# Kernel tuning notes

Measured on AMD Instinct MI355X. Metric: run time of the kernel, lower is better.

The kernel has to match this reference:

```python
import jax, jax.numpy as jnp
import numpy as np


def _count_components(img, cls):
    """Count 4-connected components of pixels equal to `cls` in a 2D int map.

    Equivalent to the numba DFS flood fill: each component is counted once.
    Implemented as min-label propagation: seed every in-class pixel with its
    linear index, iterate min over 4-neighbors (same-class only, since
    out-of-class pixels hold the sentinel BIG) until convergence; a component
    root is a pixel whose final label equals its own index.
    """
    H, W = img.shape
    BIG = H * W  # sentinel larger than any pixel index
    mask = img == cls
    idx = jnp.arange(BIG, dtype=jnp.int32).reshape(H, W)
    lab0 = jnp.where(mask, idx, BIG).astype(jnp.int32)

    def cond(state):
        return state[1]

    def body(state):
        lab, _ = state
        p = jnp.pad(lab, 1, constant_values=BIG)
        nmin = jnp.minimum(jnp.minimum(p[:-2, 1:-1], p[2:, 1:-1]),
                           jnp.minimum(p[1:-1, :-2], p[1:-1, 2:]))
        new = jnp.where(mask, jnp.minimum(lab, nmin), BIG)
        return new, jnp.any(new != lab)

    lab, _ = jax.lax.while_loop(cond, body, (lab0, jnp.array(True)))
    # roots: in-class pixels whose propagated label is their own index
    return jnp.sum(mask & (lab == idx)).astype(jnp.float32)


def _counts23(img):
    # component counts for labels 2 and 3 (the only ones the loss uses)
    return _count_components(img, 2), _count_components(img, 3)


def setup_inputs() -> dict:
    key = jax.random.key(0)
    k1, k2 = jax.random.split(key)
    pred = jax.random.normal(k1, (8, 4, 1, 768, 768), dtype=jnp.float32)
    anno = jax.random.randint(k2, (8, 1, 768, 768), 0, 4, dtype=jnp.int32)
    return {"pred": pred, "anno": anno}


def reference(pred, anno):
    # pred: [B, C, 1, H, W], anno: [B, 1, H, W]
    pred_argmax = jnp.argmax(pred, axis=1)[:, 0]  # [B, H, W] (detached semantics)
    anno_map = anno[:, 0]                          # [B, H, W]
    a2, a3 = jax.vmap(_counts23)(anno_map)
    p2, p3 = jax.vmap(_counts23)(pred_argmax)
    term2 = 1.0 - 2.0 * jnp.minimum(p2, a2) / (a2 + p2)
    term3 = 1.0 - 2.0 * jnp.minimum(p3, a3) / (a3 + p3)
    # original sums per-batch terms into connEF, then loss = connEF / 2
    return jnp.sum(term2 + term3) / 2.0
```

## Files before the change

kernel.cpp:

```cpp
#include <hip/hip_runtime.h>

#define W     768
#define PIX   (768*768)
#define NMAPS 16
#define TROWS 6
#define TPX   (TROWS*W)
#define NT    (768/TROWS)
#define NB    (NT-1)
#define NSEG  (TPX/64)
#define NIT   (NSEG/4)
#define CSLOT 16


__device__ __forceinline__ int find_root_p(volatile int* L, int x) {
    int y = L[x] >> 2;
    while (y != x) { x = y; y = L[x] >> 2; }
    return x;
}

__device__ __forceinline__ void unite_p(int* L, int a, int b, int c) {
    volatile int* Lv = L;
    while (true) {
        a = find_root_p(Lv, a);
        b = find_root_p(Lv, b);
        if (a == b) return;
        if (a > b) { int t = a; a = b; b = t; }
        int old = atomicMin(&L[b], (a << 2) | c);
        if ((old >> 2) == b) return;
        b = old >> 2;
    }
}

__device__ __forceinline__ bool unite_gp(int* L, int a, int b, int c) {
    volatile int* Lv = L;
    while (true) {
        a = find_root_p(Lv, a);
        b = find_root_p(Lv, b);
        if (a == b) return false;
        if (a > b) { int t = a; a = b; b = t; }
        int old = atomicMin(&L[b], (a << 2) | c);
        if ((old >> 2) == b) return true;
        b = old >> 2;
    }
}


__global__ __launch_bounds__(256) void fused_k(const float* __restrict__ pred,
                                               const int*   __restrict__ anno,
                                               int* __restrict__ labels,
                                               int* __restrict__ counts, int m0) {
    __shared__ int lab[TPX];
    __shared__ int s2[4], s3[4];

    int mc   = blockIdx.x / NT;
    int t    = blockIdx.x - mc * NT;
    int m    = m0 + mc;
    int tid  = threadIdx.x;
    int wid  = tid >> 6;
    int lane = tid & 63;

    unsigned long long lem = (lane == 63) ? ~0ULL : ((2ULL << lane) - 1);

    int pc[3] = {0, 0, 0};
    int pm[3] = {0, 0, 0};

    const int*   asrc = anno + (size_t)m * PIX + (size_t)t * TPX;
    const float* psrc = pred + (size_t)(m < 8 ? 0 : (m - 8)) * 4 * PIX + (size_t)t * TPX;
    bool is_anno = (m < 8);

    int   na = 0;
    float nv0 = 0.f, nv1 = 0.f, nv2 = 0.f, nv3 = 0.f;
    {
        int px = wid * 64 + lane;
        if (is_anno) {
            na = asrc[px];
        } else {
            nv0 = psrc[px];
            nv1 = psrc[(size_t)PIX + px];
            nv2 = psrc[(size_t)2 * PIX + px];
            nv3 = psrc[(size_t)3 * PIX + px];
        }
    }

    #pragma unroll
    for (int it = 0; it < NIT; ++it) {
        int seg = wid + 4 * it;
        int px  = seg * 64 + lane;
        int   ca = na;
        float v0 = nv0, v1 = nv1, v2 = nv2, v3 = nv3;
        if (it + 1 < NIT) {
            int pxn = px + 256;
            if (is_anno) {
                na = asrc[pxn];
            } else {
                nv0 = psrc[pxn];
                nv1 = psrc[(size_t)PIX + pxn];
                nv2 = psrc[(size_t)2 * PIX + pxn];
                nv3 = psrc[(size_t)3 * PIX + pxn];
            }
        }
        int c;
        if (is_anno) {
            c = ca & 3;
        } else {
            c = 0; float bv = v0;
            if (v1 > bv) { bv = v1; c = 1; }
            if (v2 > bv) { bv = v2; c = 2; }
            if (v3 > bv) { bv = v3; c = 3; }
        }
        unsigned long long blo = __ballot(c & 1);
        unsigned long long bhi = __ballot(c & 2);
        unsigned long long dif = ((blo ^ (blo << 1)) | (bhi ^ (bhi << 1))) | 1ULL;
        int ms = 63 - __clzll(dif & lem);
        lab[px] = ((seg * 64 + ms) << 2) | c;
        const int sl = it % 3;
        if (it >= 3) {
            if ((c & 2) && c == pc[sl]) {
                int mx = ms > pm[sl] ? ms : pm[sl];
                if (lane == mx) unite_p(lab, px - W, px, c);
            }
        }
        pc[sl] = c; pm[sl] = ms;
    }
    __syncthreads();

    if (tid < TROWS * 11) {
        int row = tid / 11, j = tid % 11;
        int px  = row * W + (j + 1) * 64;
        int v = lab[px], c = v & 3;
        if (c & 2) {
            int vl = lab[px - 1];
            if ((vl & 3) == c) unite_p(lab, px - 1, px, c);
        }
    }
    __syncthreads();

    int c2 = 0, c3 = 0;
    int lbase = t * TPX;
    int* gl = labels + (size_t)mc * PIX + lbase;
    #pragma unroll
    for (int it = 0; it < NIT; ++it) {
        int seg = wid + 4 * it;
        int px  = seg * 64 + lane;
        int v   = lab[px];
        int c   = v & 3;
        bool incls  = (c & 2) != 0;
        bool isroot = incls && ((v >> 2) == px);
        if (isroot) { if (c == 2) c2++; else c3++; }
        if (it < 3 || it >= NIT - 3) {
            int outv;
            if (incls) {
                int r = find_root_p(lab, px);
                outv = ((lbase + r) << 2) | c;
            } else {
                outv = ((lbase + px) << 2) | c;
            }
            gl[px] = outv;
        } else if (isroot) {
            gl[px] = ((lbase + px) << 2) | c;
        }
    }
    for (int off = 32; off; off >>= 1) {
        c2 += __shfl_down(c2, off, 64);
        c3 += __shfl_down(c3, off, 64);
    }
    if (lane == 0) { s2[wid] = c2; s3[wid] = c3; }
    __syncthreads();
    if (tid == 0) {
        int t2 = s2[0] + s2[1] + s2[2] + s2[3];
        int t3 = s3[0] + s3[1] + s3[2] + s3[3];
        if (t2) atomicAdd(&counts[(m * 2 + 0) * CSLOT], t2);
        if (t3) atomicAdd(&counts[(m * 2 + 1) * CSLOT], t3);
    }
}

__global__ __launch_bounds__(256) void boundary_k(int* __restrict__ labels,
                                                  int* __restrict__ counts, int m0) {
    __shared__ int s2[4], s3[4];
    const int HM = NB * (W / 2);
    int i    = blockIdx.x * 256 + threadIdx.x;
    int mc   = blockIdx.y;
    int m    = m0 + mc;
    int lane = threadIdx.x & 63;

    int m2 = 0, m3 = 0;
    if (i < HM) {
        int b   = i / (W / 2);
        int col = (i - b * (W / 2)) * 2;
        int* L  = labels + (size_t)mc * PIX;
        int p1  = b * TPX + (TROWS - 1) * W + col;
        int p2  = p1 + W;
        int2 va = *(const int2*)&L[p1];
        int2 vb = *(const int2*)&L[p2];
        int pay = __shfl_up(va.y, 1), pby = __shfl_up(vb.y, 1);
        int c0 = va.x & 3;
        if (c0 == (vb.x & 3) && (c0 & 2)) {
            bool red = (lane > 0) && (pay == va.x) && (pby == vb.x);
            if (!red && unite_gp(L, p1, p2, c0)) { if (c0 == 2) m2++; else m3++; }
        }
        int c1 = va.y & 3;
        if (c1 == (vb.y & 3) && (c1 & 2)) {
            bool red = (va.x == va.y) && (vb.x == vb.y);
            if (!red && unite_gp(L, p1 + 1, p2 + 1, c1)) { if (c1 == 2) m2++; else m3++; }
        }
    }
    for (int off = 32; off; off >>= 1) {
        m2 += __shfl_down(m2, off, 64);
        m3 += __shfl_down(m3, off, 64);
    }
    int wid = threadIdx.x >> 6;
    if (lane == 0) { s2[wid] = m2; s3[wid] = m3; }
    __syncthreads();
    if (threadIdx.x == 0) {
        int t2 = s2[0] + s2[1] + s2[2] + s2[3];
        int t3 = s3[0] + s3[1] + s3[2] + s3[3];
        if (t2) atomicSub(&counts[(m * 2 + 0) * CSLOT], t2);
        if (t3) atomicSub(&counts[(m * 2 + 1) * CSLOT], t3);
    }
}

__global__ void final_k(const int* __restrict__ counts, float* __restrict__ out) {
    float s = 0.0f;
    for (int b = 0; b < 8; ++b) {
        float a2 = (float)counts[(b * 2 + 0) * CSLOT];
        float a3 = (float)counts[(b * 2 + 1) * CSLOT];
        float p2 = (float)counts[((8 + b) * 2 + 0) * CSLOT];
        float p3 = (float)counts[((8 + b) * 2 + 1) * CSLOT];
        float t2 = 1.0f - 2.0f * fminf(p2, a2) / (a2 + p2);
        float t3 = 1.0f - 2.0f * fminf(p3, a3) / (a3 + p3);
        s += t2 + t3;
    }
    out[0] = 0.5f * s;
}


extern "C" void kernel_launch(void* const* d_in, const int* in_sizes, int n_in,
                              void* d_out, int out_size, void* d_ws, size_t ws_size,
                              hipStream_t stream) {
    const float* pred = (const float*)d_in[0];
    const int*   anno = (const int*)d_in[1];
    float* out = (float*)d_out;

    int* counts = (int*)d_ws;
    char* base  = (char*)d_ws + 4096;

    const size_t per_map = (size_t)PIX * 4;
    size_t avail = (ws_size > 4096) ? ws_size - 4096 : 0;
    int K = (int)(avail / per_map);
    if (K > NMAPS) K = NMAPS;
    if (K < 1)     K = 1;

    hipMemsetAsync(counts, 0, 32 * CSLOT * sizeof(int), stream);

    const int HM = NB * (W / 2);
    for (int m0 = 0; m0 < NMAPS; m0 += K) {
        int nm = NMAPS - m0; if (nm > K) nm = K;
        int* labels = (int*)base;
        fused_k   <<<dim3(nm * NT), 256, 0, stream>>>(pred, anno, labels, counts, m0);
        boundary_k<<<dim3((HM + 255) / 256, nm), 256, 0, stream>>>(labels, counts, m0);
    }
    final_k<<<1, 1, 0, stream>>>(counts, out);
}
```

Measured before the change: 57.68 us.

## Count components from run starts minus merges and write only boundary rows

Component counts are now computed during labeling: lane 0 counts the run starts of class 2 and 3 in each wavefront segment, and every successful union subtracts one. This removes the full second pass over all shared-memory pixels that looked for roots. The global label write is limited to the first and last three row-segments, plus the root entries those pixels point to. That cuts global writes, but it depends on union success being counted exactly once per merge, including under concurrent atomics.

```diff
diff --git a/kernel.cpp b/kernel.cpp
--- a/kernel.cpp
+++ b/kernel.cpp
@@ -18,20 +18,7 @@
     return x;
 }
 
-__device__ __forceinline__ void unite_p(int* L, int a, int b, int c) {
-    volatile int* Lv = L;
-    while (true) {
-        a = find_root_p(Lv, a);
-        b = find_root_p(Lv, b);
-        if (a == b) return;
-        if (a > b) { int t = a; a = b; b = t; }
-        int old = atomicMin(&L[b], (a << 2) | c);
-        if ((old >> 2) == b) return;
-        b = old >> 2;
-    }
-}
-
-__device__ __forceinline__ bool unite_gp(int* L, int a, int b, int c) {
+__device__ __forceinline__ bool unite_p(int* L, int a, int b, int c) {
     volatile int* Lv = L;
     while (true) {
         a = find_root_p(Lv, a);
@@ -63,6 +50,7 @@
 
     int pc[3] = {0, 0, 0};
     int pm[3] = {0, 0, 0};
+    int c2 = 0, c3 = 0;
 
     const int*   asrc = anno + (size_t)m * PIX + (size_t)t * TPX;
     const float* psrc = pred + (size_t)(m < 8 ? 0 : (m - 8)) * 4 * PIX + (size_t)t * TPX;
@@ -111,13 +99,19 @@
         unsigned long long blo = __ballot(c & 1);
         unsigned long long bhi = __ballot(c & 2);
         unsigned long long dif = ((blo ^ (blo << 1)) | (bhi ^ (bhi << 1))) | 1ULL;
+        if (lane == 0) {
+            c2 += (int)__popcll(dif & bhi & ~blo);
+            c3 += (int)__popcll(dif & bhi &  blo);
+        }
         int ms = 63 - __clzll(dif & lem);
         lab[px] = ((seg * 64 + ms) << 2) | c;
         const int sl = it % 3;
         if (it >= 3) {
             if ((c & 2) && c == pc[sl]) {
                 int mx = ms > pm[sl] ? ms : pm[sl];
-                if (lane == mx) unite_p(lab, px - W, px, c);
+                if (lane == mx && unite_p(lab, px - W, px, c)) {
+                    if (c == 2) c2--; else c3--;
+                }
             }
         }
         pc[sl] = c; pm[sl] = ms;
@@ -130,35 +124,28 @@
         int v = lab[px], c = v & 3;
         if (c & 2) {
             int vl = lab[px - 1];
-            if ((vl & 3) == c) unite_p(lab, px - 1, px, c);
-        }
-    }
-    __syncthreads();
-
-    int c2 = 0, c3 = 0;
+            if ((vl & 3) == c && unite_p(lab, px - 1, px, c)) {
+                if (c == 2) c2--; else c3--;
+            }
+        }
+    }
+    __syncthreads();
+
     int lbase = t * TPX;
     int* gl = labels + (size_t)mc * PIX + lbase;
     #pragma unroll
-    for (int it = 0; it < NIT; ++it) {
+    for (int q = 0; q < 6; ++q) {
+        int it  = (q < 3) ? q : (NIT - 6 + q);
         int seg = wid + 4 * it;
         int px  = seg * 64 + lane;
         int v   = lab[px];
         int c   = v & 3;
-        bool incls  = (c & 2) != 0;
-        bool isroot = incls && ((v >> 2) == px);
-        if (isroot) { if (c == 2) c2++; else c3++; }
-        if (it < 3 || it >= NIT - 3) {
-            int outv;
-            if (incls) {
-                int r = find_root_p(lab, px);
-                outv = ((lbase + r) << 2) | c;
-            } else {
-                outv = ((lbase + px) << 2) | c;
-            }
-            gl[px] = outv;
-        } else if (isroot) {
-            gl[px] = ((lbase + px) << 2) | c;
-        }
+        int r   = px;
+        if (c & 2) r = find_root_p(lab, px);
+        int rl = __shfl_up(r, 1);
+        gl[px] = ((lbase + r) << 2) | c;
+        if ((c & 2) && (lane == 0 || rl != r))
+            gl[r] = ((lbase + r) << 2) | c;
     }
     for (int off = 32; off; off >>= 1) {
         c2 += __shfl_down(c2, off, 64);
@@ -196,12 +183,12 @@
         int c0 = va.x & 3;
         if (c0 == (vb.x & 3) && (c0 & 2)) {
             bool red = (lane > 0) && (pay == va.x) && (pby == vb.x);
-            if (!red && unite_gp(L, p1, p2, c0)) { if (c0 == 2) m2++; else m3++; }
+            if (!red && unite_p(L, p1, p2, c0)) { if (c0 == 2) m2++; else m3++; }
         }
         int c1 = va.y & 3;
         if (c1 == (vb.y & 3) && (c1 & 2)) {
             bool red = (va.x == va.y) && (vb.x == vb.y);
-            if (!red && unite_gp(L, p1 + 1, p2 + 1, c1)) { if (c1 == 2) m2++; else m3++; }
+            if (!red && unite_p(L, p1 + 1, p2 + 1, c1)) { if (c1 == 2) m2++; else m3++; }
         }
     }
     for (int off = 32; off; off >>= 1) {
```

Measured after the change: 59.51 us. 3.2% more time.
